# Kernel optimization log

Hardware: AMD Instinct MI355X
Metric: run time of the kernel (lower is better)

## Reference

```python
import jax, jax.numpy as jnp
import numpy as np

B = 256          # batch of images
TOK = 256        # 16x16 tokens per image
V = 1024         # codebook size
D = 256          # code dim


def setup_inputs() -> dict:
    key = jax.random.key(0)
    k1, k2, k3, k4 = jax.random.split(key, 4)
    image_seq = jax.random.randint(k1, (B, TOK), 0, V, dtype=jnp.int64)
    image_seq2 = jax.random.randint(k2, (B, TOK), 0, V, dtype=jnp.int64)
    alpha = jax.random.uniform(k3, (1,), dtype=jnp.float32)
    W = jax.random.normal(k4, (V, D), dtype=jnp.float32)
    return {"image_seq": image_seq, "image_seq2": image_seq2, "alpha": alpha, "W": W}


def reference(image_seq, image_seq2, alpha, W):
    a = alpha[0]
    # gather codebook entries: [B, TOK, D]
    emb = W[image_seq]
    emb2 = W[image_seq2]
    x = (1.0 - a) * emb + a * emb2
    xf = x.reshape(-1, D)                        # [N, D], N = B*TOK
    # brute-force L2 distance to every code, without materializing [N, V, D]:
    d = (jnp.sum(xf * xf, axis=-1, keepdims=True)
         - 2.0 * xf @ W.T
         + jnp.sum(W * W, axis=-1)[None, :])
    idx = jnp.argmin(d, axis=1)                  # top-1 nearest code, [N]
    # get_codebook_entry: gather, reshape to bhwc, permute to bchw
    z_q = W[idx].reshape(B, 16, 16, D)           # [B, 16, 16, 256]
    z_q = jnp.transpose(z_q, (0, 3, 1, 2))       # [B, 256, 16, 16]
    return z_q
```

## Files before the change

### kernel.cpp

```cpp
#include <hip/hip_runtime.h>

static constexpr int Vn = 1024;
static constexpr int Dn = 256;
static constexpr int NT = 65536;

__global__ __launch_bounds__(256) void gram_kernel(const float* __restrict__ W,
                                                   float* __restrict__ G,
                                                   float* __restrict__ norms) {
    __shared__ float As[32][33];
    __shared__ float Bs[32][33];
    const int tid = threadIdx.x;
    const int tx = tid & 15;
    const int ty = tid >> 4;
    const int bm = blockIdx.y * 32;
    const int bn = blockIdx.x * 32;
    float acc[2][2] = {};
    for (int k0 = 0; k0 < Dn; k0 += 32) {
#pragma unroll
        for (int s = 0; s < 4; ++s) {
            const int e = tid + 256 * s;
            const int m = e >> 5;
            const int k = e & 31;
            As[k][m] = W[(bm + m) * Dn + k0 + k];
            Bs[k][m] = W[(bn + m) * Dn + k0 + k];
        }
        __syncthreads();
#pragma unroll
        for (int kk = 0; kk < 32; ++kk) {
            float a[2], b[2];
#pragma unroll
            for (int u = 0; u < 2; ++u) a[u] = As[kk][ty + 16 * u];
#pragma unroll
            for (int w = 0; w < 2; ++w) b[w] = Bs[kk][tx + 16 * w];
#pragma unroll
            for (int u = 0; u < 2; ++u)
#pragma unroll
                for (int w = 0; w < 2; ++w)
                    acc[u][w] = fmaf(a[u], b[w], acc[u][w]);
        }
        __syncthreads();
    }
#pragma unroll
    for (int u = 0; u < 2; ++u) {
        const int row = bm + ty + 16 * u;
#pragma unroll
        for (int w = 0; w < 2; ++w) {
            const int col = bn + tx + 16 * w;
            G[row * Vn + col] = acc[u][w];
            if (row == col) norms[row] = acc[u][w];
        }
    }
}

__global__ __launch_bounds__(256) void argmin_write_kernel(const int* __restrict__ seq,
                                                           const int* __restrict__ seq2,
                                                           const float* __restrict__ alpha,
                                                           const float* __restrict__ G,
                                                           const float* __restrict__ norms,
                                                           const float* __restrict__ W,
                                                           float* __restrict__ out) {
    __shared__ float nrm[Vn];
    __shared__ float T[32][257];
    __shared__ int bestVs[32];
    const int tid = threadIdx.x;
    {
        ((float4*)nrm)[tid] = ((const float4*)norms)[tid];
    }
    __syncthreads();
    const float a = alpha[0];
    const float c0 = -2.0f * (1.0f - a);
    const float c1 = -2.0f * a;
    const int wave = tid >> 6;
    const int lane = tid & 63;
    const int t0 = blockIdx.x * 32;
    const float4* nr = (const float4*)nrm;

    for (int bb = 0; bb < 2; ++bb) {
        const int base_t = t0 + wave * 8 + bb * 4;
        const int base_l = wave * 8 + bb * 4;
        int iv[4], jv[4];
#pragma unroll
        for (int q = 0; q < 4; ++q) { iv[q] = seq[base_t + q]; jv[q] = seq2[base_t + q]; }
#pragma unroll
        for (int pair = 0; pair < 2; ++pair) {
            const int qa = pair * 2, qb = pair * 2 + 1;
            const float4* GiA = (const float4*)(G + iv[qa] * Vn);
            const float4* GjA = (const float4*)(G + jv[qa] * Vn);
            const float4* GiB = (const float4*)(G + iv[qb] * Vn);
            const float4* GjB = (const float4*)(G + jv[qb] * Vn);
            float4 gia[4], gja[4], gib[4], gjb[4];
#pragma unroll
            for (int s = 0; s < 4; ++s) {
                const int e = s * 64 + lane;
                gia[s] = GiA[e];
                gja[s] = GjA[e];
                gib[s] = GiB[e];
                gjb[s] = GjB[e];
            }
            float bestA = __builtin_inff(), bestB = __builtin_inff();
            int vA = 0, vB = 0;
#pragma unroll
            for (int s = 0; s < 4; ++s) {
                const int e = s * 64 + lane;
                const float4 nn = nr[e];
                const int v = e * 4;
                {
                    const float s0 = fmaf(c1, gja[s].x, fmaf(c0, gia[s].x, nn.x));
                    const float s1 = fmaf(c1, gja[s].y, fmaf(c0, gia[s].y, nn.y));
                    const float s2 = fmaf(c1, gja[s].z, fmaf(c0, gia[s].z, nn.z));
                    const float s3 = fmaf(c1, gja[s].w, fmaf(c0, gia[s].w, nn.w));
                    if (s0 < bestA) { bestA = s0; vA = v; }
                    if (s1 < bestA) { bestA = s1; vA = v + 1; }
                    if (s2 < bestA) { bestA = s2; vA = v + 2; }
                    if (s3 < bestA) { bestA = s3; vA = v + 3; }
                }
                {
                    const float s0 = fmaf(c1, gjb[s].x, fmaf(c0, gib[s].x, nn.x));
                    const float s1 = fmaf(c1, gjb[s].y, fmaf(c0, gib[s].y, nn.y));
                    const float s2 = fmaf(c1, gjb[s].z, fmaf(c0, gib[s].z, nn.z));
                    const float s3 = fmaf(c1, gjb[s].w, fmaf(c0, gib[s].w, nn.w));
                    if (s0 < bestB) { bestB = s0; vB = v; }
                    if (s1 < bestB) { bestB = s1; vB = v + 1; }
                    if (s2 < bestB) { bestB = s2; vB = v + 2; }
                    if (s3 < bestB) { bestB = s3; vB = v + 3; }
                }
            }
#pragma unroll
            for (int off = 32; off >= 1; off >>= 1) {
                const float oa = __shfl_down(bestA, off, 64);
                const int   va = __shfl_down(vA, off, 64);
                if (oa < bestA || (oa == bestA && va < vA)) { bestA = oa; vA = va; }
                const float ob = __shfl_down(bestB, off, 64);
                const int   vb = __shfl_down(vB, off, 64);
                if (ob < bestB || (ob == bestB && vb < vB)) { bestB = ob; vB = vb; }
            }
            if (lane == 0) {
                bestVs[base_l + qa] = vA;
                bestVs[base_l + qb] = vB;
            }
        }
    }
    __syncthreads();

    const int l16 = tid & 15;
#pragma unroll
    for (int half = 0; half < 2; ++half) {
        const int tok = half * 16 + (tid >> 4);
        const int v = bestVs[tok];
        const float4* Wr = (const float4*)(W + v * Dn);
#pragma unroll
        for (int p = 0; p < 4; ++p) {
            const int d4 = p * 16 + l16;
            *(float4*)(&T[tok][d4 * 4]) = Wr[d4];
        }
    }
    __syncthreads();

    const int b   = t0 >> 8;
    const int hw0 = t0 & 255;
    float* outb = out + b * 65536 + hw0;
    const int hw = tid & 31;
    const int dofs = tid >> 5;
#pragma unroll
    for (int dp = 0; dp < 256; dp += 8) {
        const int d = dp + dofs;
        __builtin_nontemporal_store(T[hw][d], outb + d * 256 + hw);
    }
}

extern "C" void kernel_launch(void* const* d_in, const int* in_sizes, int n_in,
                              void* d_out, int out_size, void* d_ws, size_t ws_size,
                              hipStream_t stream) {
    const int*   seq   = (const int*)d_in[0];
    const int*   seq2  = (const int*)d_in[1];
    const float* alpha = (const float*)d_in[2];
    const float* W     = (const float*)d_in[3];
    float* out = (float*)d_out;

    char* ws = (char*)d_ws;
    float* G     = (float*)(ws);
    float* norms = (float*)(ws + 4194304);

    gram_kernel<<<dim3(32, 32), 256, 0, stream>>>(W, G, norms);
    argmin_write_kernel<<<NT / 32, 256, 0, stream>>>(seq, seq2, alpha, G, norms, W, out);
}
```

Measured before the change: 136.6 us.

## Keep norms in registers and write output as vectorized float4 in two halves

Each lane now loads its codebook norm values straight into registers, which removes the shared-memory norm array and one barrier. The transpose-and-write stage is split into two halves of 128 dims using a smaller shared tile. Each thread emits 16-byte nontemporal stores instead of scalar ones. The smaller shared footprint may raise occupancy and the wider stores cut store instruction count. The cost is extra barriers and scalar LDS writes when filling the tile.

```diff
diff --git a/kernel.cpp b/kernel.cpp
--- a/kernel.cpp
+++ b/kernel.cpp
@@ -3,6 +3,8 @@
 static constexpr int Vn = 1024;
 static constexpr int Dn = 256;
 static constexpr int NT = 65536;
+
+typedef float vfloat4 __attribute__((ext_vector_type(4)));
 
 __global__ __launch_bounds__(256) void gram_kernel(const float* __restrict__ W,
                                                    float* __restrict__ G,
@@ -59,21 +61,20 @@
                                                            const float* __restrict__ norms,
                                                            const float* __restrict__ W,
                                                            float* __restrict__ out) {
-    __shared__ float nrm[Vn];
-    __shared__ float T[32][257];
+    __shared__ float T[32][129];
     __shared__ int bestVs[32];
     const int tid = threadIdx.x;
-    {
-        ((float4*)nrm)[tid] = ((const float4*)norms)[tid];
-    }
-    __syncthreads();
+    const int wave = tid >> 6;
+    const int lane = tid & 63;
+    const int t0 = blockIdx.x * 32;
+
+    float4 nn_r[4];
+#pragma unroll
+    for (int s = 0; s < 4; ++s) nn_r[s] = ((const float4*)norms)[s * 64 + lane];
+
     const float a = alpha[0];
     const float c0 = -2.0f * (1.0f - a);
     const float c1 = -2.0f * a;
-    const int wave = tid >> 6;
-    const int lane = tid & 63;
-    const int t0 = blockIdx.x * 32;
-    const float4* nr = (const float4*)nrm;
 
     for (int bb = 0; bb < 2; ++bb) {
         const int base_t = t0 + wave * 8 + bb * 4;
@@ -102,7 +103,7 @@
 #pragma unroll
             for (int s = 0; s < 4; ++s) {
                 const int e = s * 64 + lane;
-                const float4 nn = nr[e];
+                const float4 nn = nn_r[s];
                 const int v = e * 4;
                 {
                     const float s0 = fmaf(c1, gja[s].x, fmaf(c0, gia[s].x, nn.x));
@@ -142,29 +143,39 @@
     }
     __syncthreads();
 
-    const int l16 = tid & 15;
-#pragma unroll
-    for (int half = 0; half < 2; ++half) {
-        const int tok = half * 16 + (tid >> 4);
-        const int v = bestVs[tok];
-        const float4* Wr = (const float4*)(W + v * Dn);
-#pragma unroll
-        for (int p = 0; p < 4; ++p) {
-            const int d4 = p * 16 + l16;
-            *(float4*)(&T[tok][d4 * 4]) = Wr[d4];
-        }
-    }
-    __syncthreads();
-
     const int b   = t0 >> 8;
     const int hw0 = t0 & 255;
     float* outb = out + b * 65536 + hw0;
-    const int hw = tid & 31;
-    const int dofs = tid >> 5;
+    const int tok = tid >> 3;
+    const int l8  = tid & 7;
+    const int hw4  = (tid & 7) * 4;
+    const int drow = tid >> 3;
 #pragma unroll
-    for (int dp = 0; dp < 256; dp += 8) {
-        const int d = dp + dofs;
-        __builtin_nontemporal_store(T[hw][d], outb + d * 256 + hw);
+    for (int half = 0; half < 2; ++half) {
+        const int v = bestVs[tok];
+        const float4* Wr = (const float4*)(W + v * Dn + half * 128);
+#pragma unroll
+        for (int p = 0; p < 4; ++p) {
+            const int d4 = p * 8 + l8;
+            const float4 w4 = Wr[d4];
+            T[tok][d4 * 4 + 0] = w4.x;
+            T[tok][d4 * 4 + 1] = w4.y;
+            T[tok][d4 * 4 + 2] = w4.z;
+            T[tok][d4 * 4 + 3] = w4.w;
+        }
+        __syncthreads();
+#pragma unroll
+        for (int dp = 0; dp < 128; dp += 32) {
+            const int dl = dp + drow;
+            const int d = half * 128 + dl;
+            vfloat4 o;
+            o.x = T[hw4 + 0][dl];
+            o.y = T[hw4 + 1][dl];
+            o.z = T[hw4 + 2][dl];
+            o.w = T[hw4 + 3][dl];
+            __builtin_nontemporal_store(o, (vfloat4*)(outb + d * 256 + hw4));
+        }
+        __syncthreads();
     }
 }
 
```

Result: faster. 130.4 us (-4.5%).
